# Kernel tuning notes

Measured on AMD Instinct MI355X. Metric: run time of the kernel, lower is better.

The kernel has to match this reference:

```python
import jax, jax.numpy as jnp
import numpy as np

N_EXPERTS = 6
TOP_K = 2
IN_DIM, HID_DIM, OUT_DIM = 1024, 4096, 1024
N_TOKENS = 8192


def setup_inputs() -> dict:
    key = jax.random.key(0)
    ks = jax.random.split(key, 7)
    s_in = 1.0 / np.sqrt(IN_DIM)
    s_hid = 1.0 / np.sqrt(HID_DIM)
    return {
        "x": jax.random.normal(ks[0], (N_TOKENS, IN_DIM), dtype=jnp.float32),
        "Wg": jax.random.uniform(ks[1], (IN_DIM, N_EXPERTS), jnp.float32, -s_in, s_in),
        "bg": jax.random.uniform(ks[2], (N_EXPERTS,), jnp.float32, -s_in, s_in),
        "W1": jax.random.uniform(ks[3], (N_EXPERTS, IN_DIM, HID_DIM), jnp.float32, -s_in, s_in),
        "b1": jax.random.uniform(ks[4], (N_EXPERTS, HID_DIM), jnp.float32, -s_in, s_in),
        "W2": jax.random.uniform(ks[5], (N_EXPERTS, HID_DIM, OUT_DIM), jnp.float32, -s_hid, s_hid),
        "b2": jax.random.uniform(ks[6], (N_EXPERTS, OUT_DIM), jnp.float32, -s_hid, s_hid),
    }


def reference(x, Wg, bg, W1, b1, W2, b2):
    n_experts = Wg.shape[-1]
    # gating: scores [N, E]
    scores = x @ Wg + bg
    _, topk_idx = jax.lax.top_k(scores, TOP_K)  # [N, k]
    # binary mask of selected experts [N, E]
    mask = jax.nn.one_hot(topk_idx, n_experts, dtype=scores.dtype).sum(axis=1)
    weights = jax.nn.softmax(scores, axis=-1) * mask
    weights = weights / (weights.sum(axis=-1, keepdims=True) + 1e-8)
    # dense all-expert compute (faithful to original): hidden [N, E, H]
    h = jax.nn.relu(jnp.einsum("ni,eih->neh", x, W1) + b1)
    outputs = jnp.einsum("neh,eho->neo", h, W2) + b2  # [N, E, O]
    return jnp.einsum("ne,neo->no", weights, outputs)
```

## Files before the change

kernel.cpp:

```cpp
#include <hip/hip_runtime.h>

typedef unsigned short u16;
typedef float f32x4 __attribute__((ext_vector_type(4)));
typedef __bf16 bf16x8 __attribute__((ext_vector_type(8)));
typedef unsigned short u16x8 __attribute__((ext_vector_type(8)));
typedef unsigned short u16x4 __attribute__((ext_vector_type(4)));
typedef unsigned long long ull;

#define N_TOKENS 8192
#define IN_DIM   1024
#define HID_DIM  4096
#define OUT_DIM  1024
#define N_EXP    6

__device__ __forceinline__ u16 f2bf(float f) {
  union { float f; unsigned int u; } v; v.f = f;
  unsigned int u = v.u;
  unsigned int r = (u + 0x7FFFu + ((u >> 16) & 1u)) >> 16;
  return (u16)r;
}

__device__ __forceinline__ float bf2f(u16 v) {
  union { unsigned int u; float f; } x; x.u = ((unsigned int)v) << 16; return x.f;
}

__device__ __forceinline__ void load_lds16(const void* g, void* l) {
  __builtin_amdgcn_global_load_lds(
      (const __attribute__((address_space(1))) void*)g,
      (__attribute__((address_space(3))) void*)l, 16, 0, 0);
}

__global__ __launch_bounds__(256) void transpose_cvt2(const float* __restrict__ W1,
                                                      const float* __restrict__ W2,
                                                      u16* __restrict__ W1T,
                                                      u16* __restrict__ W2T) {
  const float* src; u16* dst; int R, C;
  if (blockIdx.z == 0) { src = W1; dst = W1T; R = IN_DIM; C = HID_DIM; }
  else                 { src = W2; dst = W2T; R = HID_DIM; C = OUT_DIM; }
  const size_t esz = (size_t)R * C;
  src += (size_t)blockIdx.y * esz;
  dst += (size_t)blockIdx.y * esz;
  const int tiles_x = C / 64;
  const int tx = blockIdx.x % tiles_x, ty = blockIdx.x / tiles_x;
  __shared__ u16 tile[64][72];
  int c0 = tx * 64, r0 = ty * 64;
  int t = threadIdx.x;
  int cc = (t & 15) * 4, rb = t >> 4;
#pragma unroll
  for (int p = 0; p < 4; p++) {
    int r = p * 16 + rb;
    float4 v = *(const float4*)(src + (size_t)(r0 + r) * C + c0 + cc);
    tile[cc + 0][r] = f2bf(v.x);
    tile[cc + 1][r] = f2bf(v.y);
    tile[cc + 2][r] = f2bf(v.z);
    tile[cc + 3][r] = f2bf(v.w);
  }
  __syncthreads();
  int c = t >> 2, rp = (t & 3) * 16;
  u16* dp = dst + (size_t)(c0 + c) * R + r0 + rp;
  *(u16x8*)(dp)     = *(const u16x8*)&tile[c][rp];
  *(u16x8*)(dp + 8) = *(const u16x8*)&tile[c][rp + 8];
}

__global__ __launch_bounds__(256) void gating_kernel(const float* __restrict__ x,
                                                     const float* __restrict__ Wg,
                                                     const float* __restrict__ bg,
                                                     u16* __restrict__ xb,
                                                     int* __restrict__ gate_e,
                                                     float* __restrict__ gate_w) {
  int lane = threadIdx.x & 63, wid = threadIdx.x >> 6;
  int tok = blockIdx.x * 4 + wid;
  float acc[N_EXP] = {0.f, 0.f, 0.f, 0.f, 0.f, 0.f};
  const float4* xr = (const float4*)(x + (size_t)tok * IN_DIM);
  u16* xw = xb + (size_t)tok * IN_DIM;
#pragma unroll
  for (int g = 0; g < 4; g++) {
    float4 v = xr[lane + g * 64];
    int c0 = (lane + g * 64) * 4;
    u16x4 o; o[0] = f2bf(v.x); o[1] = f2bf(v.y); o[2] = f2bf(v.z); o[3] = f2bf(v.w);
    *(u16x4*)(xw + c0) = o;
#pragma unroll
    for (int c = 0; c < 4; c++) {
      float xv = (c == 0) ? v.x : (c == 1) ? v.y : (c == 2) ? v.z : v.w;
      const float* wr = Wg + (c0 + c) * N_EXP;
#pragma unroll
      for (int e = 0; e < N_EXP; e++) acc[e] += xv * wr[e];
    }
  }
#pragma unroll
  for (int e = 0; e < N_EXP; e++) {
    float a = acc[e];
#pragma unroll
    for (int off = 32; off > 0; off >>= 1) a += __shfl_xor(a, off, 64);
    acc[e] = a;
  }
  if (lane == 0) {
    float s[N_EXP];
#pragma unroll
    for (int e = 0; e < N_EXP; e++) s[e] = acc[e] + bg[e];
    float mx = s[0];
#pragma unroll
    for (int e = 1; e < N_EXP; e++) mx = fmaxf(mx, s[e]);
    float p[N_EXP], sum = 0.f;
#pragma unroll
    for (int e = 0; e < N_EXP; e++) { p[e] = expf(s[e] - mx); sum += p[e]; }
    int a = 0;
#pragma unroll
    for (int e = 1; e < N_EXP; e++) if (s[e] > s[a]) a = e;
    int b = (a == 0) ? 1 : 0;
#pragma unroll
    for (int e = 0; e < N_EXP; e++) if (e != a && s[e] > s[b]) b = e;
    float pa = p[a] / sum, pb = p[b] / sum;
    float den = pa + pb + 1e-8f;
    gate_e[2 * tok] = a; gate_e[2 * tok + 1] = b;
    gate_w[2 * tok] = pa / den; gate_w[2 * tok + 1] = pb / den;
  }
}

__global__ __launch_bounds__(384) void routing_kernel(const int* __restrict__ gate_e,
                                                      int* __restrict__ idxl,
                                                      int* __restrict__ tokslot,
                                                      int* __restrict__ meta) {
  int wave = threadIdx.x >> 6, lane = threadIdx.x & 63;
  __shared__ int s_cnt[N_EXP];
  if (wave < N_EXP) {
    const int e = wave;
    int cnt = 0;
    const int4* gp = (const int4*)gate_e;
    int4 g = gp[lane];
    const ull below = (1ull << lane) - 1ull;
    for (int it = 0; it < N_TOKENS / 128; it++) {
      int4 gn;
      if (it + 1 < N_TOKENS / 128) gn = gp[(it + 1) * 64 + lane];
      bool s0 = (g.x == e) || (g.y == e);
      bool s1 = (g.z == e) || (g.w == e);
      ull m0 = __ballot(s0), m1 = __ballot(s1);
      int p0 = __popcll(m0 & below) + __popcll(m1 & below);
      int t0 = it * 128 + 2 * lane;
      if (s0) {
        int j = cnt + p0;
        idxl[e * N_TOKENS + j] = t0;
        tokslot[2 * t0 + ((g.x == e) ? 0 : 1)] = j;
      }
      if (s1) {
        int j = cnt + p0 + (s0 ? 1 : 0);
        idxl[e * N_TOKENS + j] = t0 + 1;
        tokslot[2 * (t0 + 1) + ((g.z == e) ? 0 : 1)] = j;
      }
      cnt += __popcll(m0) + __popcll(m1);
      g = gn;
    }
    if (lane == 0) s_cnt[e] = cnt;
  }
  __syncthreads();
  if (threadIdx.x == 0) {
    int off = 0;
    for (int e = 0; e < N_EXP; e++) { meta[e] = s_cnt[e]; meta[8 + e] = off; off += s_cnt[e]; }
    meta[8 + N_EXP] = off;
  }
}


#define GDS_A(AH) \
  _Pragma("unroll") for (int mi = 0; mi < 4; mi++) { \
    int r_ = (AH)*128 + wr*64 + mi*16 + lrow; \
    af[mi][0] = *(const bf16x8*)&sA[cur][r_*64 + ((lhi ^ lx7) * 8)]; \
    af[mi][1] = *(const bf16x8*)&sA[cur][r_*64 + (((4 + lhi) ^ lx7) * 8)]; }

#define GDS_B(BH) \
  _Pragma("unroll") for (int nj = 0; nj < 2; nj++) { \
    int r_ = (BH)*128 + wc*32 + nj*16 + lrow; \
    bfr[nj][0] = *(const bf16x8*)&sB[cur][r_*64 + ((lhi ^ lx7) * 8)]; \
    bfr[nj][1] = *(const bf16x8*)&sB[cur][r_*64 + (((4 + lhi) ^ lx7) * 8)]; }

#define GSTG_A(HH) \
  load_lds16(pa[HH][0] + ksn, &sA[nxt][((HH)*128 + wave*16) * 64]); \
  load_lds16(pa[HH][1] + ksn, &sA[nxt][((HH)*128 + wave*16 + 8) * 64]);

#define GSTG_B(HH) \
  load_lds16(pb[HH][0] + ksn, &sB[nxt][((HH)*128 + wave*16) * 64]); \
  load_lds16(pb[HH][1] + ksn, &sB[nxt][((HH)*128 + wave*16 + 8) * 64]);

#define GMFMA_Q(AH, BH) \
  _Pragma("unroll") for (int mi = 0; mi < 4; mi++) \
  _Pragma("unroll") for (int nj = 0; nj < 2; nj++) { \
    acc[AH][BH][mi][nj] = __builtin_amdgcn_mfma_f32_16x16x32_bf16(af[mi][0], bfr[nj][0], acc[AH][BH][mi][nj], 0, 0, 0); \
    acc[AH][BH][mi][nj] = __builtin_amdgcn_mfma_f32_16x16x32_bf16(af[mi][1], bfr[nj][1], acc[AH][BH][mi][nj], 0, 0, 0); }

#define GBAR __builtin_amdgcn_s_barrier()
#define GLGKM0 asm volatile("s_waitcnt lgkmcnt(0)" ::: "memory")
#define GVMC(n) asm volatile("s_waitcnt vmcnt(" #n ")" ::: "memory")

#define GEMM_KLOOP(NT_)                                                        \
  { const int ksn = 0; const int nxt = 0;                                      \
    GSTG_A(0); GSTG_B(0); GSTG_A(1); GSTG_B(1); }                              \
  GVMC(4);                                                                     \
  GBAR;                                                                        \
  int cur = 0;                                                                 \
  for (int t = 0; t < (NT_); t++) {                                            \
    const int nxt = cur ^ 1;                                                   \
    const int ksn = ((t + 1 < (NT_)) ? (t + 1) : ((NT_) - 1)) * 64;            \
                                                          \
    GDS_A(0); GDS_B(0);                                                        \
    GSTG_A(0);                                                                 \
    GBAR; GLGKM0;                                                              \
    __builtin_amdgcn_s_setprio(1); GMFMA_Q(0, 0); __builtin_amdgcn_s_setprio(0); \
    GVMC(2); GBAR;                                                             \
                                                          \
    GDS_B(1);                                                                  \
    GSTG_B(0);                                                                 \
    GBAR; GLGKM0;                                                              \
    __builtin_amdgcn_s_setprio(1); GMFMA_Q(0, 1); __builtin_amdgcn_s_setprio(0); \
    GBAR;                                                                      \
                                                          \
    GDS_A(1); GDS_B(0);                                                        \
    GSTG_A(1);                                                                 \
    GBAR; GLGKM0;                                                              \
    __builtin_amdgcn_s_setprio(1); GMFMA_Q(1, 0); __builtin_amdgcn_s_setprio(0); \
    GBAR;                                                                      \
                                                          \
    GDS_B(1);                                                                  \
    GSTG_B(1);                                                                 \
    GBAR; GLGKM0;                                                              \
    __builtin_amdgcn_s_setprio(1); GMFMA_Q(1, 1); __builtin_amdgcn_s_setprio(0); \
    GVMC(4); GBAR;                                                             \
    cur = nxt;                                                                 \
  }

__device__ __forceinline__ void decode_expert(const int* meta, int mtg,
                                              int& e, int& mt, int& cnt) {
  e = -1; mt = 0; cnt = 0;
  int sum = 0;
#pragma unroll
  for (int ee = 0; ee < N_EXP; ee++) {
    int c = meta[ee];
    int nt = (c + 255) >> 8;
    if (e < 0 && mtg < sum + nt) { e = ee; mt = mtg - sum; cnt = c; }
    sum += nt;
  }
}

__global__ __launch_bounds__(512) void gemm1_kernel(const u16* __restrict__ xb,
                                                    const u16* __restrict__ W1T,
                                                    const float* __restrict__ b1,
                                                    const int* __restrict__ idxl,
                                                    const int* __restrict__ meta,
                                                    u16* __restrict__ h) {
  __shared__ u16 sA[2][16384];
  __shared__ u16 sB[2][16384];
  const int bid = blockIdx.x;
  const int xcd = bid & 7;
  const int s = bid >> 3;
  const int chunk = s / 36, q = s % 36;
  const int n = chunk * 4 + (q & 3);
  const int mtg = xcd * 9 + (q >> 2);

  int e, mt, cnt;
  decode_expert(meta, mtg, e, mt, cnt);
  if (e < 0) return;
  const int off = meta[8 + e];
  const int bn0 = n * 256;
  const int tid = threadIdx.x, lane = tid & 63, wave = tid >> 6;
  const int wr = wave >> 2, wc = wave & 3;
  const int lrow = lane & 15, lhi = lane >> 4, lx7 = lane & 7;
  const int schunk = (lane & 7) ^ (lane >> 3);

  const u16* pa[2][2];
  const u16* pb[2][2];
  const u16* bbase = W1T + (size_t)e * HID_DIM * IN_DIM;
#pragma unroll
  for (int hh = 0; hh < 2; hh++)
#pragma unroll
    for (int i = 0; i < 2; i++) {
      int gr = hh * 128 + wave * 16 + i * 8 + (lane >> 3);
      int j = mt * 256 + gr; if (j >= cnt) j = cnt - 1;
      int tok = idxl[e * N_TOKENS + j];
      pa[hh][i] = xb + (size_t)tok * IN_DIM + schunk * 8;
      pb[hh][i] = bbase + (size_t)(bn0 + gr) * IN_DIM + schunk * 8;
    }

  f32x4 acc[2][2][4][2] = {};
  bf16x8 af[4][2], bfr[2][2];

  GEMM_KLOOP(IN_DIM / 64)

#pragma unroll
  for (int ah = 0; ah < 2; ah++)
#pragma unroll
    for (int bh = 0; bh < 2; bh++)
#pragma unroll
      for (int nj = 0; nj < 2; nj++) {
        int col = bn0 + bh * 128 + wc * 32 + nj * 16 + lrow;
        float bias = b1[e * HID_DIM + col];
#pragma unroll
        for (int mi = 0; mi < 4; mi++)
#pragma unroll
          for (int rr = 0; rr < 4; rr++) {
            int j = mt * 256 + ah * 128 + wr * 64 + mi * 16 + lhi * 4 + rr;
            if (j < cnt) {
              float v = fmaxf(acc[ah][bh][mi][nj][rr] + bias, 0.f);
              h[(size_t)(off + j) * HID_DIM + col] = f2bf(v);
            }
          }
      }
}

__global__ __launch_bounds__(512) void gemm2_kernel(const u16* __restrict__ hbuf,
                                                    const u16* __restrict__ W2T,
                                                    const float* __restrict__ b2,
                                                    const int* __restrict__ meta,
                                                    u16* __restrict__ y0,
                                                    u16* __restrict__ y1) {
  __shared__ u16 sA[2][16384];
  __shared__ u16 sB[2][16384];
  const int bid = blockIdx.x;
  const int xcd = bid & 7;
  const int s = bid >> 3;
  const int v = s & 7;
  const int mtg = xcd * 9 + (s >> 3);
  const int n = v >> 1, kzid = v & 1;

  int e, mt, cnt;
  decode_expert(meta, mtg, e, mt, cnt);
  if (e < 0) return;
  const int off = meta[8 + e];
  const int bn0 = n * 256;
  const int kz = kzid * (HID_DIM / 2);
  const int tid = threadIdx.x, lane = tid & 63, wave = tid >> 6;
  const int wr = wave >> 2, wc = wave & 3;
  const int lrow = lane & 15, lhi = lane >> 4, lx7 = lane & 7;
  const int schunk = (lane & 7) ^ (lane >> 3);

  const u16* pa[2][2];
  const u16* pb[2][2];
  const u16* bbase = W2T + (size_t)e * OUT_DIM * HID_DIM;
#pragma unroll
  for (int hh = 0; hh < 2; hh++)
#pragma unroll
    for (int i = 0; i < 2; i++) {
      int gr = hh * 128 + wave * 16 + i * 8 + (lane >> 3);
      int j = mt * 256 + gr; if (j >= cnt) j = cnt - 1;
      pa[hh][i] = hbuf + (size_t)(off + j) * HID_DIM + kz + schunk * 8;
      pb[hh][i] = bbase + (size_t)(bn0 + gr) * HID_DIM + kz + schunk * 8;
    }

  f32x4 acc[2][2][4][2] = {};
  bf16x8 af[4][2], bfr[2][2];

  GEMM_KLOOP(HID_DIM / 2 / 64)

  u16* __restrict__ yb = kzid ? y1 : y0;
#pragma unroll
  for (int ah = 0; ah < 2; ah++)
#pragma unroll
    for (int bh = 0; bh < 2; bh++)
#pragma unroll
      for (int nj = 0; nj < 2; nj++) {
        int col = bn0 + bh * 128 + wc * 32 + nj * 16 + lrow;
        float bias = (kzid == 0) ? b2[e * OUT_DIM + col] : 0.f;
#pragma unroll
        for (int mi = 0; mi < 4; mi++)
#pragma unroll
          for (int rr = 0; rr < 4; rr++) {
            int j = mt * 256 + ah * 128 + wr * 64 + mi * 16 + lhi * 4 + rr;
            if (j < cnt)
              yb[(size_t)(off + j) * OUT_DIM + col] = f2bf(acc[ah][bh][mi][nj][rr] + bias);
          }
      }
}

__global__ __launch_bounds__(256) void combine_kernel(const u16* __restrict__ y0,
                                                      const u16* __restrict__ y1,
                                                      const int* __restrict__ gate_e,
                                                      const float* __restrict__ gate_w,
                                                      const int* __restrict__ tokslot,
                                                      const int* __restrict__ meta,
                                                      float* __restrict__ out) {
  const int t = blockIdx.x;
  const int e0 = gate_e[2 * t], e1 = gate_e[2 * t + 1];
  const float w0 = gate_w[2 * t], w1 = gate_w[2 * t + 1];
  const size_t s0 = (size_t)(meta[8 + e0] + tokslot[2 * t]) * OUT_DIM;
  const size_t s1 = (size_t)(meta[8 + e1] + tokslot[2 * t + 1]) * OUT_DIM;
  const int c = threadIdx.x * 4;
  u16x4 a0 = *(const u16x4*)(y0 + s0 + c);
  u16x4 b0 = *(const u16x4*)(y1 + s0 + c);
  u16x4 a1 = *(const u16x4*)(y0 + s1 + c);
  u16x4 b1 = *(const u16x4*)(y1 + s1 + c);
  float4 o;
  o.x = w0 * (bf2f(a0[0]) + bf2f(b0[0])) + w1 * (bf2f(a1[0]) + bf2f(b1[0]));
  o.y = w0 * (bf2f(a0[1]) + bf2f(b0[1])) + w1 * (bf2f(a1[1]) + bf2f(b1[1]));
  o.z = w0 * (bf2f(a0[2]) + bf2f(b0[2])) + w1 * (bf2f(a1[2]) + bf2f(b1[2]));
  o.w = w0 * (bf2f(a0[3]) + bf2f(b0[3])) + w1 * (bf2f(a1[3]) + bf2f(b1[3]));
  *(float4*)(out + (size_t)t * OUT_DIM + c) = o;
}

extern "C" void kernel_launch(void* const* d_in, const int* in_sizes, int n_in,
                              void* d_out, int out_size, void* d_ws, size_t ws_size,
                              hipStream_t stream) {
  const float* x  = (const float*)d_in[0];
  const float* Wg = (const float*)d_in[1];
  const float* bg = (const float*)d_in[2];
  const float* W1 = (const float*)d_in[3];
  const float* b1 = (const float*)d_in[4];
  const float* W2 = (const float*)d_in[5];
  const float* b2 = (const float*)d_in[6];
  float* out = (float*)d_out;

  char* ws = (char*)d_ws;
  u16*   xb     = (u16*)(ws);
  u16*   W1T    = (u16*)(ws + 16777216);
  u16*   y0     = (u16*)(ws);
  u16*   y1     = (u16*)(ws + 33554432);
  u16*   W2T    = (u16*)(ws + 67108864);
  u16*   h      = (u16*)(ws + 117440512);
  int*   gate_e = (int*)(ws + 251658240);
  float* gate_w = (float*)(ws + 251723776);
  int*   idxl   = (int*)(ws + 251789312);
  int*   tokslot= (int*)(ws + 251985920);
  int*   meta   = (int*)(ws + 252051456);

  transpose_cvt2<<<dim3(1024, N_EXP, 2), 256, 0, stream>>>(W1, W2, W1T, W2T);
  gating_kernel<<<2048, 256, 0, stream>>>(x, Wg, bg, xb, gate_e, gate_w);
  routing_kernel<<<1, 384, 0, stream>>>(gate_e, idxl, tokslot, meta);
  gemm1_kernel<<<1152, 512, 0, stream>>>(xb, W1T, b1, idxl, meta, h);
  gemm2_kernel<<<576, 512, 0, stream>>>(h, W2T, b2, meta, y0, y1);
  combine_kernel<<<N_TOKENS, 256, 0, stream>>>(y0, y1, gate_e, gate_w, tokslot, meta, out);
}
```

Before: 547.7 us.

## Gather routed tokens into contiguous buffer and fuse W1 transpose with gating

Adds a gather kernel that copies each expert's routed token rows into a contiguous bf16 buffer, so gemm1 reads A rows linearly instead of through the idxl indirection. The W1 transpose/convert is merged with gating into one prep kernel. The W2 transpose is split out and launched after gemm1 so its output can reuse workspace memory. The cost is an extra launch and an extra pass over the gathered activations (about 32 MB of bf16).

```diff
diff --git a/kernel.cpp b/kernel.cpp
--- a/kernel.cpp
+++ b/kernel.cpp
@@ -30,20 +30,13 @@
       (__attribute__((address_space(3))) void*)l, 16, 0, 0);
 }
 
-__global__ __launch_bounds__(256) void transpose_cvt2(const float* __restrict__ W1,
-                                                      const float* __restrict__ W2,
-                                                      u16* __restrict__ W1T,
-                                                      u16* __restrict__ W2T) {
-  const float* src; u16* dst; int R, C;
-  if (blockIdx.z == 0) { src = W1; dst = W1T; R = IN_DIM; C = HID_DIM; }
-  else                 { src = W2; dst = W2T; R = HID_DIM; C = OUT_DIM; }
+__global__ __launch_bounds__(256) void transpose_cvt(const float* __restrict__ src,
+                                                     u16* __restrict__ dst, int R, int C) {
+  __shared__ u16 tile[64][72];
   const size_t esz = (size_t)R * C;
-  src += (size_t)blockIdx.y * esz;
-  dst += (size_t)blockIdx.y * esz;
-  const int tiles_x = C / 64;
-  const int tx = blockIdx.x % tiles_x, ty = blockIdx.x / tiles_x;
-  __shared__ u16 tile[64][72];
-  int c0 = tx * 64, r0 = ty * 64;
+  src += (size_t)blockIdx.z * esz;
+  dst += (size_t)blockIdx.z * esz;
+  int c0 = blockIdx.x * 64, r0 = blockIdx.y * 64;
   int t = threadIdx.x;
   int cc = (t & 15) * 4, rb = t >> 4;
 #pragma unroll
@@ -62,14 +55,44 @@
   *(u16x8*)(dp + 8) = *(const u16x8*)&tile[c][rp + 8];
 }
 
-__global__ __launch_bounds__(256) void gating_kernel(const float* __restrict__ x,
-                                                     const float* __restrict__ Wg,
-                                                     const float* __restrict__ bg,
-                                                     u16* __restrict__ xb,
-                                                     int* __restrict__ gate_e,
-                                                     float* __restrict__ gate_w) {
+__global__ __launch_bounds__(256) void prep_kernel(const float* __restrict__ W1,
+                                                   u16* __restrict__ W1T,
+                                                   const float* __restrict__ x,
+                                                   const float* __restrict__ Wg,
+                                                   const float* __restrict__ bg,
+                                                   u16* __restrict__ xb,
+                                                   int* __restrict__ gate_e,
+                                                   float* __restrict__ gate_w) {
+  __shared__ u16 tile[64][72];
+  const int bid = blockIdx.x;
+  if (bid < 6144) {
+    const int ex = bid >> 10, ti = bid & 1023;
+    const float* src = W1 + (size_t)ex * IN_DIM * HID_DIM;
+    u16* dst = W1T + (size_t)ex * IN_DIM * HID_DIM;
+    const int tx = ti & 63, ty = ti >> 6;
+    const int C = HID_DIM, R = IN_DIM;
+    int c0 = tx * 64, r0 = ty * 64;
+    int t = threadIdx.x;
+    int cc = (t & 15) * 4, rb = t >> 4;
+#pragma unroll
+    for (int p = 0; p < 4; p++) {
+      int r = p * 16 + rb;
+      float4 v = *(const float4*)(src + (size_t)(r0 + r) * C + c0 + cc);
+      tile[cc + 0][r] = f2bf(v.x);
+      tile[cc + 1][r] = f2bf(v.y);
+      tile[cc + 2][r] = f2bf(v.z);
+      tile[cc + 3][r] = f2bf(v.w);
+    }
+    __syncthreads();
+    int c = t >> 2, rp = (t & 3) * 16;
+    u16* dp = dst + (size_t)(c0 + c) * R + r0 + rp;
+    *(u16x8*)(dp)     = *(const u16x8*)&tile[c][rp];
+    *(u16x8*)(dp + 8) = *(const u16x8*)&tile[c][rp + 8];
+    return;
+  }
+  const int gb = bid - 6144;
   int lane = threadIdx.x & 63, wid = threadIdx.x >> 6;
-  int tok = blockIdx.x * 4 + wid;
+  int tok = gb * 4 + wid;
   float acc[N_EXP] = {0.f, 0.f, 0.f, 0.f, 0.f, 0.f};
   const float4* xr = (const float4*)(x + (size_t)tok * IN_DIM);
   u16* xw = xb + (size_t)tok * IN_DIM;
@@ -160,6 +183,20 @@
   }
 }
 
+__global__ __launch_bounds__(256) void gather_kernel(const u16* __restrict__ xb,
+                                                     const int* __restrict__ idxl,
+                                                     const int* __restrict__ meta,
+                                                     u16* __restrict__ xg) {
+  const int s = blockIdx.x * 2 + (threadIdx.x >> 7);
+  const int c = (threadIdx.x & 127) * 8;
+  int e = 0;
+#pragma unroll
+  for (int ee = 1; ee < N_EXP; ee++) if (s >= meta[8 + ee]) e = ee;
+  const int j = s - meta[8 + e];
+  const int tok = idxl[e * N_TOKENS + j];
+  *(u16x8*)(xg + (size_t)s * IN_DIM + c) = *(const u16x8*)(xb + (size_t)tok * IN_DIM + c);
+}
+
 
 #define GDS_A(AH) \
   _Pragma("unroll") for (int mi = 0; mi < 4; mi++) { \
@@ -240,10 +277,9 @@
   }
 }
 
-__global__ __launch_bounds__(512) void gemm1_kernel(const u16* __restrict__ xb,
+__global__ __launch_bounds__(512) void gemm1_kernel(const u16* __restrict__ xg,
                                                     const u16* __restrict__ W1T,
                                                     const float* __restrict__ b1,
-                                                    const int* __restrict__ idxl,
                                                     const int* __restrict__ meta,
                                                     u16* __restrict__ h) {
   __shared__ u16 sA[2][16384];
@@ -274,8 +310,7 @@
     for (int i = 0; i < 2; i++) {
       int gr = hh * 128 + wave * 16 + i * 8 + (lane >> 3);
       int j = mt * 256 + gr; if (j >= cnt) j = cnt - 1;
-      int tok = idxl[e * N_TOKENS + j];
-      pa[hh][i] = xb + (size_t)tok * IN_DIM + schunk * 8;
+      pa[hh][i] = xg + (size_t)(off + j) * IN_DIM + schunk * 8;
       pb[hh][i] = bbase + (size_t)(bn0 + gr) * IN_DIM + schunk * 8;
     }
 
@@ -407,22 +442,24 @@
   float* out = (float*)d_out;
 
   char* ws = (char*)d_ws;
-  u16*   xb     = (u16*)(ws);
-  u16*   W1T    = (u16*)(ws + 16777216);
-  u16*   y0     = (u16*)(ws);
-  u16*   y1     = (u16*)(ws + 33554432);
-  u16*   W2T    = (u16*)(ws + 67108864);
-  u16*   h      = (u16*)(ws + 117440512);
+  u16*   h      = (u16*)(ws);
+  u16*   xg     = (u16*)(ws + 134217728);
+  u16*   W1T    = (u16*)(ws + 167772160);
+  u16*   W2T    = (u16*)(ws + 134217728);
+  u16*   xb     = (u16*)(ws + 218103808);
+  u16*   y0     = (u16*)(ws + 184549376);
+  u16*   y1     = (u16*)(ws + 218103808);
   int*   gate_e = (int*)(ws + 251658240);
   float* gate_w = (float*)(ws + 251723776);
   int*   idxl   = (int*)(ws + 251789312);
   int*   tokslot= (int*)(ws + 251985920);
   int*   meta   = (int*)(ws + 252051456);
 
-  transpose_cvt2<<<dim3(1024, N_EXP, 2), 256, 0, stream>>>(W1, W2, W1T, W2T);
-  gating_kernel<<<2048, 256, 0, stream>>>(x, Wg, bg, xb, gate_e, gate_w);
+  prep_kernel<<<8192, 256, 0, stream>>>(W1, W1T, x, Wg, bg, xb, gate_e, gate_w);
   routing_kernel<<<1, 384, 0, stream>>>(gate_e, idxl, tokslot, meta);
-  gemm1_kernel<<<1152, 512, 0, stream>>>(xb, W1T, b1, idxl, meta, h);
+  gather_kernel<<<N_TOKENS, 256, 0, stream>>>(xb, idxl, meta, xg);
+  gemm1_kernel<<<1152, 512, 0, stream>>>(xg, W1T, b1, meta, h);
+  transpose_cvt<<<dim3(OUT_DIM / 64, HID_DIM / 64, N_EXP), 256, 0, stream>>>(W2, W2T, HID_DIM, OUT_DIM);
   gemm2_kernel<<<576, 512, 0, stream>>>(h, W2T, b2, meta, y0, y1);
   combine_kernel<<<N_TOKENS, 256, 0, stream>>>(y0, y1, gate_e, gate_w, tokslot, meta, out);
 }
```

New measurement: 559.6 us. 2.2% more time.

## Fuse W1 transpose with gating and overlap W2 transpose with gemm1

Applied to the files above, without the earlier changes.

Merges the W1 transpose/convert and the gating kernel into a single prep launch. The W2 transpose/convert moves into extra blocks appended to the gemm1 grid, so that memory-bound conversion work can fill the machine alongside the compute-bound GEMM tiles. This cuts launches and the serialization between the prep stages. In exchange the W2 blocks launch after the GEMM blocks, and the gemm1 kernel's register and LDS footprint now applies to the simple transpose blocks too.

```diff
diff --git a/kernel.cpp b/kernel.cpp
--- a/kernel.cpp
+++ b/kernel.cpp
@@ -30,46 +30,44 @@
       (__attribute__((address_space(3))) void*)l, 16, 0, 0);
 }
 
-__global__ __launch_bounds__(256) void transpose_cvt2(const float* __restrict__ W1,
-                                                      const float* __restrict__ W2,
-                                                      u16* __restrict__ W1T,
-                                                      u16* __restrict__ W2T) {
-  const float* src; u16* dst; int R, C;
-  if (blockIdx.z == 0) { src = W1; dst = W1T; R = IN_DIM; C = HID_DIM; }
-  else                 { src = W2; dst = W2T; R = HID_DIM; C = OUT_DIM; }
-  const size_t esz = (size_t)R * C;
-  src += (size_t)blockIdx.y * esz;
-  dst += (size_t)blockIdx.y * esz;
-  const int tiles_x = C / 64;
-  const int tx = blockIdx.x % tiles_x, ty = blockIdx.x / tiles_x;
+__global__ __launch_bounds__(256) void prep_kernel(const float* __restrict__ W1,
+                                                   u16* __restrict__ W1T,
+                                                   const float* __restrict__ x,
+                                                   const float* __restrict__ Wg,
+                                                   const float* __restrict__ bg,
+                                                   u16* __restrict__ xb,
+                                                   int* __restrict__ gate_e,
+                                                   float* __restrict__ gate_w) {
   __shared__ u16 tile[64][72];
-  int c0 = tx * 64, r0 = ty * 64;
-  int t = threadIdx.x;
-  int cc = (t & 15) * 4, rb = t >> 4;
-#pragma unroll
-  for (int p = 0; p < 4; p++) {
-    int r = p * 16 + rb;
-    float4 v = *(const float4*)(src + (size_t)(r0 + r) * C + c0 + cc);
-    tile[cc + 0][r] = f2bf(v.x);
-    tile[cc + 1][r] = f2bf(v.y);
-    tile[cc + 2][r] = f2bf(v.z);
-    tile[cc + 3][r] = f2bf(v.w);
-  }
-  __syncthreads();
-  int c = t >> 2, rp = (t & 3) * 16;
-  u16* dp = dst + (size_t)(c0 + c) * R + r0 + rp;
-  *(u16x8*)(dp)     = *(const u16x8*)&tile[c][rp];
-  *(u16x8*)(dp + 8) = *(const u16x8*)&tile[c][rp + 8];
-}
-
-__global__ __launch_bounds__(256) void gating_kernel(const float* __restrict__ x,
-                                                     const float* __restrict__ Wg,
-                                                     const float* __restrict__ bg,
-                                                     u16* __restrict__ xb,
-                                                     int* __restrict__ gate_e,
-                                                     float* __restrict__ gate_w) {
+  const int bid = blockIdx.x;
+  if (bid < 6144) {
+    const int ex = bid >> 10, ti = bid & 1023;
+    const float* src = W1 + (size_t)ex * IN_DIM * HID_DIM;
+    u16* dst = W1T + (size_t)ex * IN_DIM * HID_DIM;
+    const int tx = ti & 63, ty = ti >> 6;
+    const int C = HID_DIM, R = IN_DIM;
+    int c0 = tx * 64, r0 = ty * 64;
+    int t = threadIdx.x;
+    int cc = (t & 15) * 4, rb = t >> 4;
+#pragma unroll
+    for (int p = 0; p < 4; p++) {
+      int r = p * 16 + rb;
+      float4 v = *(const float4*)(src + (size_t)(r0 + r) * C + c0 + cc);
+      tile[cc + 0][r] = f2bf(v.x);
+      tile[cc + 1][r] = f2bf(v.y);
+      tile[cc + 2][r] = f2bf(v.z);
+      tile[cc + 3][r] = f2bf(v.w);
+    }
+    __syncthreads();
+    int c = t >> 2, rp = (t & 3) * 16;
+    u16* dp = dst + (size_t)(c0 + c) * R + r0 + rp;
+    *(u16x8*)(dp)     = *(const u16x8*)&tile[c][rp];
+    *(u16x8*)(dp + 8) = *(const u16x8*)&tile[c][rp + 8];
+    return;
+  }
+  const int gb = bid - 6144;
   int lane = threadIdx.x & 63, wid = threadIdx.x >> 6;
-  int tok = blockIdx.x * 4 + wid;
+  int tok = gb * 4 + wid;
   float acc[N_EXP] = {0.f, 0.f, 0.f, 0.f, 0.f, 0.f};
   const float4* xr = (const float4*)(x + (size_t)tok * IN_DIM);
   u16* xw = xb + (size_t)tok * IN_DIM;
@@ -245,10 +243,38 @@
                                                     const float* __restrict__ b1,
                                                     const int* __restrict__ idxl,
                                                     const int* __restrict__ meta,
-                                                    u16* __restrict__ h) {
+                                                    u16* __restrict__ h,
+                                                    const float* __restrict__ W2,
+                                                    u16* __restrict__ W2T) {
   __shared__ u16 sA[2][16384];
   __shared__ u16 sB[2][16384];
   const int bid = blockIdx.x;
+  if (bid >= 1152) {
+    u16 (*tile)[72] = (u16(*)[72])&sA[0][0];
+    const int ti = bid - 1152;
+    const int ex = ti >> 10;
+    const int t2 = ti & 1023;
+    const int tx = t2 & 15, ty = t2 >> 4;
+    const float* src = W2 + (size_t)ex * HID_DIM * OUT_DIM;
+    u16* dst = W2T + (size_t)ex * HID_DIM * OUT_DIM;
+    const int C = OUT_DIM, R = HID_DIM;
+    const int c0 = tx * 64, r0 = ty * 64;
+    const int t = threadIdx.x;
+    const int cc = (t & 15) * 4, rb = t >> 4;
+#pragma unroll
+    for (int p = 0; p < 2; p++) {
+      int r = p * 32 + rb;
+      float4 v = *(const float4*)(src + (size_t)(r0 + r) * C + c0 + cc);
+      tile[cc + 0][r] = f2bf(v.x);
+      tile[cc + 1][r] = f2bf(v.y);
+      tile[cc + 2][r] = f2bf(v.z);
+      tile[cc + 3][r] = f2bf(v.w);
+    }
+    __syncthreads();
+    const int c = t >> 3, rp = (t & 7) * 8;
+    *(u16x8*)(dst + (size_t)(c0 + c) * R + r0 + rp) = *(const u16x8*)&tile[c][rp];
+    return;
+  }
   const int xcd = bid & 7;
   const int s = bid >> 3;
   const int chunk = s / 36, q = s % 36;
@@ -419,10 +445,9 @@
   int*   tokslot= (int*)(ws + 251985920);
   int*   meta   = (int*)(ws + 252051456);
 
-  transpose_cvt2<<<dim3(1024, N_EXP, 2), 256, 0, stream>>>(W1, W2, W1T, W2T);
-  gating_kernel<<<2048, 256, 0, stream>>>(x, Wg, bg, xb, gate_e, gate_w);
+  prep_kernel<<<8192, 256, 0, stream>>>(W1, W1T, x, Wg, bg, xb, gate_e, gate_w);
   routing_kernel<<<1, 384, 0, stream>>>(gate_e, idxl, tokslot, meta);
-  gemm1_kernel<<<1152, 512, 0, stream>>>(xb, W1T, b1, idxl, meta, h);
+  gemm1_kernel<<<7296, 512, 0, stream>>>(xb, W1T, b1, idxl, meta, h, W2, W2T);
   gemm2_kernel<<<576, 512, 0, stream>>>(h, W2T, b2, meta, y0, y1);
   combine_kernel<<<N_TOKENS, 256, 0, stream>>>(y0, y1, gate_e, gate_w, tokslot, meta, out);
 }
```

Measured after the change: 532.9 us, median of 2. 1.03x faster.
